# Optimization experiments

Measured on AMD Instinct MI355X. Metric: run time of the kernel, lower is better.

## Reference

```python
import jax, jax.numpy as jnp
import numpy as np

N = 4096      # nodes
E = 131072    # edges (before self loops)
C = 512       # channels
H = 8         # heads
CO = C // H   # per-head out channels (64)
EPS = 1e-5
NEG_SLOPE = 0.2


def layer_norm(x, g, b):
    mu = jnp.mean(x, axis=-1, keepdims=True)
    var = jnp.mean((x - mu) ** 2, axis=-1, keepdims=True)
    return (x - mu) * jax.lax.rsqrt(var + EPS) * g + b


def gatv2(x, src, dst, wl, bl, wr, br, att, bias):
    # PyG GATv2Conv, concat=True, add_self_loops handled by caller.
    n = x.shape[0]
    xl = (x @ wl.T + bl).reshape(n, H, CO)   # target-side features
    xr = (x @ wr.T + br).reshape(n, H, CO)   # source-side features (messages)
    e = jax.nn.leaky_relu(xl[dst] + xr[src], NEG_SLOPE)   # [E+N, H, CO]
    alpha = jnp.einsum('ehc,hc->eh', e, att)              # [E+N, H]
    # segment softmax over destination neighborhoods
    amax = jax.ops.segment_max(alpha, dst, num_segments=n)
    ex = jnp.exp(alpha - amax[dst])
    denom = jax.ops.segment_sum(ex, dst, num_segments=n)
    a = ex / denom[dst]                                   # [E+N, H]
    msg = xr[src] * a[:, :, None]                         # [E+N, H, CO]
    out = jax.ops.segment_sum(msg, dst, num_segments=n)   # [N, H, CO]
    return out.reshape(n, H * CO) + bias


def mha(x, in_w, in_b, out_w, out_b):
    # nn.MultiheadAttention self-attention, batch=1, eval mode
    n = x.shape[0]
    qkv = x @ in_w.T + in_b                               # [N, 3C]
    q, k, v = jnp.split(qkv, 3, axis=-1)
    q = q.reshape(n, H, CO); k = k.reshape(n, H, CO); v = v.reshape(n, H, CO)
    scores = jnp.einsum('qhd,khd->hqk', q, k) / jnp.sqrt(jnp.float32(CO))
    p = jax.nn.softmax(scores, axis=-1)
    o = jnp.einsum('hqk,khd->qhd', p, v).reshape(n, C)
    return o @ out_w.T + out_b


def setup_inputs() -> dict:
    key = jax.random.key(0)
    ks = jax.random.split(key, 24)
    s = 0.02
    d = {}
    d['x'] = jax.random.normal(ks[0], (N, C), jnp.float32)
    d['edge_index'] = jax.random.randint(ks[1], (2, E), 0, N, dtype=jnp.int64)
    d['gat_wl'] = jax.random.normal(ks[2], (H * CO, C), jnp.float32) * s
    d['gat_bl'] = jnp.zeros((H * CO,), jnp.float32)
    d['gat_wr'] = jax.random.normal(ks[3], (H * CO, C), jnp.float32) * s
    d['gat_br'] = jnp.zeros((H * CO,), jnp.float32)
    d['gat_att'] = jax.random.normal(ks[4], (H, CO), jnp.float32) * s
    d['gat_b'] = jnp.zeros((H * CO,), jnp.float32)
    d['in_w'] = jax.random.normal(ks[5], (3 * C, C), jnp.float32) * s
    d['in_b'] = jnp.zeros((3 * C,), jnp.float32)
    d['out_w'] = jax.random.normal(ks[6], (C, C), jnp.float32) * s
    d['out_b'] = jnp.zeros((C,), jnp.float32)
    d['ln1_g'] = jnp.ones((C,), jnp.float32); d['ln1_b'] = jnp.zeros((C,), jnp.float32)
    d['ln2_g'] = jnp.ones((C,), jnp.float32); d['ln2_b'] = jnp.zeros((C,), jnp.float32)
    d['ln3_g'] = jnp.ones((C,), jnp.float32); d['ln3_b'] = jnp.zeros((C,), jnp.float32)
    d['w1'] = jax.random.normal(ks[7], (4 * C, C), jnp.float32) * s
    d['b1'] = jnp.zeros((4 * C,), jnp.float32)
    d['w2'] = jax.random.normal(ks[8], (C, 4 * C), jnp.float32) * s
    d['b2'] = jnp.zeros((C,), jnp.float32)
    return d


def reference(x, edge_index, gat_wl, gat_bl, gat_wr, gat_br, gat_att, gat_b,
              in_w, in_b, out_w, out_b, ln1_g, ln1_b, ln2_g, ln2_b,
              ln3_g, ln3_b, w1, b1, w2, b2):
    n = x.shape[0]
    loops = jnp.arange(n, dtype=edge_index.dtype)
    src = jnp.concatenate([edge_index[0], loops])
    dst = jnp.concatenate([edge_index[1], loops])
    h_local = gatv2(x, src, dst, gat_wl, gat_bl, gat_wr, gat_br, gat_att, gat_b)
    x = layer_norm(x + h_local, ln1_g, ln1_b)
    h_global = mha(x, in_w, in_b, out_w, out_b)
    x = layer_norm(x + h_global, ln2_g, ln2_b)
    h_ffn = (jax.nn.gelu(x @ w1.T + b1, approximate=False)) @ w2.T + b2
    x = layer_norm(x + h_ffn, ln3_g, ln3_b)
    return x
```

## Files before the change

kernel.cpp:

```cpp
#include <hip/hip_runtime.h>
#include <math.h>

#define NN 4096
#define CC 512
#define EE 131072
#define NEDGE (EE + NN)
#define HH 8
#define DCO 64
#define NC2 2097152L

typedef __attribute__((ext_vector_type(8))) short bfrag;
typedef __attribute__((ext_vector_type(4))) float f32x4;
typedef __attribute__((ext_vector_type(4))) int i32x4;

__device__ __forceinline__ float bf2f(unsigned short u) {
  union { float f; unsigned int i; } x; x.i = ((unsigned int)u) << 16; return x.f;
}
__device__ __forceinline__ unsigned short f2bf(float f) {
  union { float f; unsigned int i; } x; x.f = f;
  unsigned int r = x.i + 0x7FFFu + ((x.i >> 16) & 1u);
  return (unsigned short)(r >> 16);
}
__device__ __forceinline__ unsigned short f2bf_trunc(float f) {
  union { float f; unsigned int i; } x; x.f = f;
  return (unsigned short)(x.i >> 16);
}

__device__ __forceinline__ void gld16(const unsigned short* g, unsigned short* l) {
  __builtin_amdgcn_global_load_lds(
      (__attribute__((address_space(1))) unsigned int*)g,
      (__attribute__((address_space(3))) unsigned int*)l, 16, 0, 0);
}

#define QSC 0.18033688011112042f

#define CX  2097152L
#define CWL (CX + 262144L)
#define CWR (CWL + 262144L)
#define CIW (CWR + 786432L)
#define COW (CIW + 262144L)
#define CW1 (COW + 1048576L)
#define CW2 (CW1 + 1048576L)

__global__ void cvt_all(const float* __restrict__ x, const float* __restrict__ wl,
                        const float* __restrict__ wr, const float* __restrict__ iw,
                        const float* __restrict__ ow, const float* __restrict__ w1,
                        const float* __restrict__ w2, unsigned short* __restrict__ dst,
                        int* __restrict__ cntcur, const float* __restrict__ bl,
                        const float* __restrict__ br, float* __restrict__ biasc) {
  if (blockIdx.x >= 5632) {
    int t = threadIdx.x;
    if (blockIdx.x == 5632) {
      for (int k = t; k < 8192; k += 256) cntcur[k] = 0;
    } else {
      for (int k = t; k < 512; k += 256) {
        biasc[k] = bl[k];
        biasc[512 + k] = br[k];
      }
    }
    return;
  }
  long i = ((long)blockIdx.x * 256 + threadIdx.x) * 4;
  const float* s; long o;
  if (i < CX)       { s = x;  o = i; }
  else if (i < CWL) { s = wl; o = i - CX; }
  else if (i < CWR) { s = wr; o = i - CWL; }
  else if (i < CIW) { s = iw; o = i - CWR; }
  else if (i < COW) { s = ow; o = i - CIW; }
  else if (i < CW1) { s = w1; o = i - COW; }
  else              { s = w2; o = i - CW1; }
  f32x4 v = *(const f32x4*)(s + o);
  union { unsigned long long q; unsigned short u[4]; } t;
#pragma unroll
  for (int j = 0; j < 4; j++) t.u[j] = f2bf(v[j]);
  *(unsigned long long*)(dst + i) = t.q;
}

template<int OMODE, int TN, bool SPLIT>
__global__ __launch_bounds__(256) void gemm_t(
    const unsigned short* __restrict__ A, const unsigned short* __restrict__ B,
    const float* __restrict__ bias, void* __restrict__ C,
    int K, int lda, int ldb, int ldc)
{
  __shared__ unsigned short As[4096];
  __shared__ unsigned short Bs[TN * 32];
  constexpr int MI = (TN == 128) ? 4 : 2;
  const int tid = threadIdx.x;
  const int wave = tid >> 6, lane = tid & 63;
  const int ml = lane & 15, kq = lane >> 4;
  const int wm = (TN == 128) ? ((wave >> 1) << 6) : (wave << 5);
  const int wn = (TN == 128) ? ((wave & 1) << 6) : 0;
  const int bm = blockIdx.y << 7, bn = blockIdx.x * TN;
  const int srow = tid >> 2, scol = (tid & 3) << 3;
  if (SPLIT) { A += (long)blockIdx.z * K; B += (long)blockIdx.z * K; }
  const float* biasp = (!SPLIT || blockIdx.z == 0) ? bias : nullptr;
  const unsigned short* Ag = A + (long)(bm + srow) * lda + scol;
  const unsigned short* Bg = B + (long)(bn + srow) * ldb + scol;
  const long astep = (long)64 * lda, bstep = (long)64 * ldb;
  unsigned short* lA0 = As + tid * 8;
  unsigned short* lA1 = As + 2048 + tid * 8;
  unsigned short* lB0 = Bs + tid * 8;
  f32x4 acc[MI][4];
#pragma unroll
  for (int mi = 0; mi < MI; mi++)
#pragma unroll
    for (int ni = 0; ni < 4; ni++) acc[mi][ni] = (f32x4){0.f, 0.f, 0.f, 0.f};
  for (int k0 = 0; k0 < K; k0 += 32) {
    __syncthreads();
    gld16(Ag, lA0); gld16(Ag + astep, lA1);
    gld16(Bg, lB0);
    if (TN == 128) gld16(Bg + bstep, Bs + 2048 + tid * 8);
    Ag += 32; Bg += 32;
    __syncthreads();
    bfrag af[MI], bf[4];
#pragma unroll
    for (int mi = 0; mi < MI; mi++)
      af[mi] = *(const bfrag*)&As[(wm + (mi << 4) + ml) * 32 + (kq << 3)];
#pragma unroll
    for (int ni = 0; ni < 4; ni++)
      bf[ni] = *(const bfrag*)&Bs[(wn + (ni << 4) + ml) * 32 + (kq << 3)];
#pragma unroll
    for (int mi = 0; mi < MI; mi++)
#pragma unroll
      for (int ni = 0; ni < 4; ni++)
        acc[mi][ni] = __builtin_amdgcn_mfma_f32_16x16x32_bf16(af[mi], bf[ni], acc[mi][ni], 0, 0, 0);
  }
#pragma unroll
  for (int ni = 0; ni < 4; ni++) {
    int col = bn + wn + (ni << 4) + ml;
    float bb = biasp ? biasp[col] : 0.f;
#pragma unroll
    for (int mi = 0; mi < MI; mi++) {
      int row0 = bm + wm + (mi << 4) + (kq << 2);
#pragma unroll
      for (int r = 0; r < 4; r++) {
        float v = acc[mi][ni][r] + bb;
        int row = row0 + r;
        if (OMODE == 3) {
          unsigned short* q = (unsigned short*)C;
          if (col < 512) {
            int h = col >> 6, d = col & 63;
            q[(long)h * (NN * DCO) + (long)row * DCO + d] = f2bf(v * QSC);
          } else if (col < 1024) {
            int c2 = col - 512, h = c2 >> 6, d = c2 & 63;
            q[NC2 + (long)h * (NN * DCO) + (long)row * DCO + d] = f2bf(v);
          } else {
            int c2 = col - 1024, h = c2 >> 6, d = c2 & 63;
            q[2 * NC2 + (long)h * (DCO * NN) + (long)d * NN + row] = f2bf(v);
          }
        } else if (OMODE == 0) {
          long off = (SPLIT ? (long)blockIdx.z * NC2 : 0) + (long)row * ldc + col;
          ((float*)C)[off] = v;
        } else {
          if (OMODE == 2) v = 0.5f * v * (1.f + erff(v * 0.70710678118f));
          ((unsigned short*)C)[(long)row * ldc + col] = f2bf(v);
        }
      }
    }
  }
}

__global__ void count_k(const int* __restrict__ ei, int* __restrict__ cnt) {
  int e = blockIdx.x * 256 + threadIdx.x;
  if (e >= NEDGE) return;
  int d = (e < EE) ? ei[EE + e] : (e - EE);
  atomicAdd(&cnt[d], 1);
}

__global__ void scan_k(const int* __restrict__ cnt, int* __restrict__ rowptr) {
  __shared__ int s[1024];
  int t = threadIdx.x;
  int b = t * 4;
  int c0 = cnt[b], c1 = cnt[b + 1], c2 = cnt[b + 2], c3 = cnt[b + 3];
  int sum = c0 + c1 + c2 + c3;
  s[t] = sum;
  __syncthreads();
  for (int o = 1; o < 1024; o <<= 1) {
    int v = (t >= o) ? s[t - o] : 0;
    __syncthreads();
    s[t] += v;
    __syncthreads();
  }
  int ex = s[t] - sum;
  rowptr[b] = ex; rowptr[b + 1] = ex + c0;
  rowptr[b + 2] = ex + c0 + c1; rowptr[b + 3] = ex + c0 + c1 + c2;
  if (t == 1023) rowptr[4096] = ex + sum;
}

__global__ void scatter_k(const int* __restrict__ ei, const int* __restrict__ rowptr,
                          int* __restrict__ cur, int* __restrict__ order) {
  int e = blockIdx.x * 256 + threadIdx.x;
  if (e >= NEDGE) return;
  int d = (e < EE) ? ei[EE + e] : (e - EE);
  int p = atomicAdd(&cur[d], 1);
  order[rowptr[d] + p] = e;
}

__global__ __launch_bounds__(256) void gat_fused(
    const unsigned short* __restrict__ xlr, const float* __restrict__ x,
    const int* __restrict__ order, const int* __restrict__ rowptr,
    const int* __restrict__ ei, const float* __restrict__ att,
    const float* __restrict__ gbias,
    const float* __restrict__ g, const float* __restrict__ be,
    float* __restrict__ of, unsigned short* __restrict__ ob)
{
  __shared__ float part[4][512];
  __shared__ float sw[4][8];
  __shared__ float sinv[8];
  __shared__ float shl[8];
  int n = blockIdx.x, t = threadIdx.x;
  int beg = rowptr[n], deg = rowptr[n + 1] - beg;
  int wave = t >> 6, lane = t & 63;
  int ch = lane << 3;
  union U8 { i32x4 v; unsigned short u[8]; };
  U8 XL; XL.v = *(const i32x4*)(xlr + (long)n * 1024 + ch);
  float xl[8];
#pragma unroll
  for (int j = 0; j < 8; j++) xl[j] = bf2f(XL.u[j]);
  f32x4 t0 = *(const f32x4*)(att + ch);
  f32x4 t1 = *(const f32x4*)(att + ch + 4);
  float acc[8];
#pragma unroll
  for (int j = 0; j < 8; j++) acc[j] = 0.f;
  float se = 0.f;
  int i = wave;
  U8 X;
  if (i < deg) {
    int e = order[beg + i];
    int sn = (e < EE) ? ei[e] : (e - EE);
    X.v = *(const i32x4*)(xlr + (long)sn * 1024 + 512 + ch);
  }
  while (i < deg) {
    U8 Xc = X;
    int inext = i + 4;
    if (inext < deg) {
      int e = order[beg + inext];
      int sn = (e < EE) ? ei[e] : (e - EE);
      X.v = *(const i32x4*)(xlr + (long)sn * 1024 + 512 + ch);
    }
    float xr[8];
    float p = 0.f;
#pragma unroll
    for (int j = 0; j < 8; j++) {
      xr[j] = bf2f(Xc.u[j]);
      float v = xl[j] + xr[j];
      v = (v > 0.f) ? v : 0.2f * v;
      float tv = (j < 4) ? t0[j] : t1[j - 4];
      p += tv * v;
    }
    p += __shfl_xor(p, 1); p += __shfl_xor(p, 2); p += __shfl_xor(p, 4);
    float ew = __expf(p);
    se += ew;
#pragma unroll
    for (int j = 0; j < 8; j++) acc[j] += ew * xr[j];
    i = inext;
  }
  *(f32x4*)&part[wave][ch]     = (f32x4){acc[0], acc[1], acc[2], acc[3]};
  *(f32x4*)&part[wave][ch + 4] = (f32x4){acc[4], acc[5], acc[6], acc[7]};
  if ((lane & 7) == 0) sw[wave][lane >> 3] = se;
  __syncthreads();
  if (t < 8) sinv[t] = 1.f / (sw[0][t] + sw[1][t] + sw[2][t] + sw[3][t]);
  __syncthreads();
  long base = (long)n * CC;
  float v0, v1;
  {
    int c = t;
    float p4 = part[0][c] + part[1][c] + part[2][c] + part[3][c];
    v0 = x[base + c] + p4 * sinv[c >> 6] + gbias[c];
  }
  {
    int c = t + 256;
    float p4 = part[0][c] + part[1][c] + part[2][c] + part[3][c];
    v1 = x[base + c] + p4 * sinv[c >> 6] + gbias[c];
  }
  float s = v0 + v1, ss = v0 * v0 + v1 * v1;
  for (int o = 32; o > 0; o >>= 1) { s += __shfl_down(s, o); ss += __shfl_down(ss, o); }
  if (lane == 0) { shl[wave] = s; shl[4 + wave] = ss; }
  __syncthreads();
  float S = shl[0] + shl[1] + shl[2] + shl[3];
  float SS = shl[4] + shl[5] + shl[6] + shl[7];
  float mean = S * (1.f / 512.f);
  float var = SS * (1.f / 512.f) - mean * mean;
  float rs = rsqrtf(var + 1e-5f);
  float y0 = (v0 - mean) * rs * g[t] + be[t];
  float y1 = (v1 - mean) * rs * g[t + 256] + be[t + 256];
  of[base + t] = y0; of[base + t + 256] = y1;
  ob[base + t] = f2bf(y0); ob[base + t + 256] = f2bf(y1);
}

template<int NS>
__global__ __launch_bounds__(256) void resid_ln(
    const float* __restrict__ a, const float* __restrict__ b,
    const float* __restrict__ g, const float* __restrict__ be,
    float* __restrict__ of, unsigned short* __restrict__ ob)
{
  __shared__ float sh[8];
  int row = blockIdx.x, t = threadIdx.x;
  long base = (long)row * CC;
  float b0 = 0.f, b1 = 0.f;
#pragma unroll
  for (int s = 0; s < NS; s++) {
    b0 += b[(long)s * NC2 + base + t];
    b1 += b[(long)s * NC2 + base + t + 256];
  }
  float v0 = a[base + t] + b0;
  float v1 = a[base + t + 256] + b1;
  float s = v0 + v1, ss = v0 * v0 + v1 * v1;
  for (int o = 32; o > 0; o >>= 1) { s += __shfl_down(s, o); ss += __shfl_down(ss, o); }
  int wave = t >> 6, lane = t & 63;
  if (lane == 0) { sh[wave] = s; sh[4 + wave] = ss; }
  __syncthreads();
  float S = sh[0] + sh[1] + sh[2] + sh[3];
  float SS = sh[4] + sh[5] + sh[6] + sh[7];
  float mean = S * (1.f / 512.f);
  float var = SS * (1.f / 512.f) - mean * mean;
  float rs = rsqrtf(var + 1e-5f);
  float y0 = (v0 - mean) * rs * g[t] + be[t];
  float y1 = (v1 - mean) * rs * g[t + 256] + be[t + 256];
  if (of) { of[base + t] = y0; of[base + t + 256] = y1; }
  if (ob) { ob[base + t] = f2bf(y0); ob[base + t + 256] = f2bf(y1); }
}

__global__ __launch_bounds__(256, 4) void flash_attn(
    const unsigned short* __restrict__ qkvP, unsigned short* __restrict__ Op,
    float* __restrict__ Lp)
{
  __shared__ unsigned short QP[128 * 72];
  __shared__ unsigned short Ks[64 * 72];
  __shared__ unsigned short Vs[64 * 72];
  const int tid = threadIdx.x;
  const int wave = tid >> 6, lane = tid & 63;
  const int ml = lane & 15, kq = lane >> 4;
  const int h = blockIdx.x & 7, qt = blockIdx.x >> 3;
  const int sp = blockIdx.y;
  const int n0 = qt << 7;
  const unsigned short* Qh = qkvP + (long)h * (NN * DCO);
  const unsigned short* Kh = qkvP + NC2 + (long)h * (NN * DCO);
  const unsigned short* Vh = qkvP + 2 * NC2 + (long)h * (DCO * NN);
  {
    int r = tid >> 1, c = (tid & 1) << 5;
    const unsigned short* src = Qh + (long)(n0 + r) * DCO + c;
    unsigned short* d = &QP[r * 72 + c];
    *(i32x4*)d        = *(const i32x4*)src;
    *(i32x4*)(d + 8)  = *(const i32x4*)(src + 8);
    *(i32x4*)(d + 16) = *(const i32x4*)(src + 16);
    *(i32x4*)(d + 24) = *(const i32x4*)(src + 24);
  }
  __syncthreads();
  bfrag aq[2][2];
#pragma unroll
  for (int s = 0; s < 2; s++)
#pragma unroll
    for (int kh = 0; kh < 2; kh++)
      aq[s][kh] = *(const bfrag*)&QP[(wave * 32 + s * 16 + ml) * 72 + kh * 32 + (kq << 3)];
  bfrag ones;
#pragma unroll
  for (int j = 0; j < 8; j++) ones[j] = (short)0x3F80;
  f32x4 Oa[2][4];
  f32x4 Lc[2];
#pragma unroll
  for (int s = 0; s < 2; s++) {
    Lc[s] = (f32x4){0.f, 0.f, 0.f, 0.f};
#pragma unroll
    for (int dg = 0; dg < 4; dg++) Oa[s][dg] = (f32x4){0.f, 0.f, 0.f, 0.f};
  }
  const int r_ = tid >> 2, c_ = (tid & 3) << 4;
  const int j0 = sp << 4;
  i32x4 ka, kb, va, vb;
  {
    int k0 = j0 << 6;
    ka = *(const i32x4*)(Kh + (long)(k0 + r_) * DCO + c_);
    kb = *(const i32x4*)(Kh + (long)(k0 + r_) * DCO + c_ + 8);
    va = *(const i32x4*)(Vh + (long)r_ * NN + k0 + c_);
    vb = *(const i32x4*)(Vh + (long)r_ * NN + k0 + c_ + 8);
  }
  for (int jj = 0; jj < 16; jj++) {
    if (jj) __syncthreads();
    *(i32x4*)&Ks[r_ * 72 + c_] = ka; *(i32x4*)&Ks[r_ * 72 + c_ + 8] = kb;
    *(i32x4*)&Vs[r_ * 72 + c_] = va; *(i32x4*)&Vs[r_ * 72 + c_ + 8] = vb;
    __syncthreads();
    if (jj < 15) {
      int k0 = (j0 + jj + 1) << 6;
      ka = *(const i32x4*)(Kh + (long)(k0 + r_) * DCO + c_);
      kb = *(const i32x4*)(Kh + (long)(k0 + r_) * DCO + c_ + 8);
      va = *(const i32x4*)(Vh + (long)r_ * NN + k0 + c_);
      vb = *(const i32x4*)(Vh + (long)r_ * NN + k0 + c_ + 8);
    }
    f32x4 sc[2][4];
#pragma unroll
    for (int s = 0; s < 2; s++)
#pragma unroll
      for (int c = 0; c < 4; c++) sc[s][c] = (f32x4){0.f, 0.f, 0.f, 0.f};
    __builtin_amdgcn_s_setprio(1);
#pragma unroll
    for (int c = 0; c < 4; c++) {
      bfrag bk0 = *(const bfrag*)&Ks[(c * 16 + ml) * 72 + (kq << 3)];
      bfrag bk1 = *(const bfrag*)&Ks[(c * 16 + ml) * 72 + 32 + (kq << 3)];
#pragma unroll
      for (int s = 0; s < 2; s++) {
        sc[s][c] = __builtin_amdgcn_mfma_f32_16x16x32_bf16(bk0, aq[s][0], sc[s][c], 0, 0, 0);
        sc[s][c] = __builtin_amdgcn_mfma_f32_16x16x32_bf16(bk1, aq[s][1], sc[s][c], 0, 0, 0);
      }
    }
    __builtin_amdgcn_s_setprio(0);
#pragma unroll
    for (int s = 0; s < 2; s++) {
#pragma unroll
      for (int c = 0; c < 4; c++) {
        float p0 = exp2f(sc[s][c][0]);
        float p1 = exp2f(sc[s][c][1]);
        float p2 = exp2f(sc[s][c][2]);
        float p3 = exp2f(sc[s][c][3]);
        unsigned int w0, w1;
        asm("v_cvt_pk_bf16_f32 %0, %1, %2" : "=v"(w0) : "v"(p0), "v"(p1));
        asm("v_cvt_pk_bf16_f32 %0, %1, %2" : "=v"(w1) : "v"(p2), "v"(p3));
        union { unsigned long long q; unsigned int w[2]; } u;
        u.w[0] = w0; u.w[1] = w1;
        *(unsigned long long*)&QP[(wave * 32 + s * 16 + ml) * 72 + c * 16 + (kq << 2)] = u.q;
      }
    }
    bfrag ap[2][2];
#pragma unroll
    for (int s = 0; s < 2; s++)
#pragma unroll
      for (int kh = 0; kh < 2; kh++)
        ap[s][kh] = *(const bfrag*)&QP[(wave * 32 + s * 16 + ml) * 72 + kh * 32 + (kq << 3)];
    __builtin_amdgcn_s_setprio(1);
#pragma unroll
    for (int s = 0; s < 2; s++) {
      Lc[s] = __builtin_amdgcn_mfma_f32_16x16x32_bf16(ap[s][0], ones, Lc[s], 0, 0, 0);
      Lc[s] = __builtin_amdgcn_mfma_f32_16x16x32_bf16(ap[s][1], ones, Lc[s], 0, 0, 0);
    }
#pragma unroll
    for (int dg = 0; dg < 4; dg++) {
      bfrag bv0 = *(const bfrag*)&Vs[(dg * 16 + ml) * 72 + (kq << 3)];
      bfrag bv1 = *(const bfrag*)&Vs[(dg * 16 + ml) * 72 + 32 + (kq << 3)];
#pragma unroll
      for (int s = 0; s < 2; s++) {
        Oa[s][dg] = __builtin_amdgcn_mfma_f32_16x16x32_bf16(ap[s][0], bv0, Oa[s][dg], 0, 0, 0);
        Oa[s][dg] = __builtin_amdgcn_mfma_f32_16x16x32_bf16(ap[s][1], bv1, Oa[s][dg], 0, 0, 0);
      }
    }
    __builtin_amdgcn_s_setprio(0);
  }
  long obase = (long)sp * NC2;
#pragma unroll
  for (int s = 0; s < 2; s++)
#pragma unroll
    for (int dg = 0; dg < 4; dg++)
#pragma unroll
      for (int r = 0; r < 4; r++) {
        int row = wave * 32 + s * 16 + (kq << 2) + r;
        Op[obase + (long)(n0 + row) * CC + (h << 6) + (dg << 4) + ml] = f2bf(Oa[s][dg][r]);
      }
  if (ml == 0) {
#pragma unroll
    for (int s = 0; s < 2; s++)
#pragma unroll
      for (int r = 0; r < 4; r++) {
        int row = wave * 32 + s * 16 + (kq << 2) + r;
        Lp[(long)sp * (NN * HH) + (long)(n0 + row) * HH + h] = Lc[s][r];
      }
  }
}

__global__ void flash_combine(const unsigned short* __restrict__ Op,
                              const float* __restrict__ Lp,
                              unsigned short* __restrict__ Ao) {
  int idx = blockIdx.x * 256 + threadIdx.x;
  int n = idx >> 9, c = idx & 511, h = c >> 6;
  float l = 0.f, o = 0.f;
#pragma unroll
  for (int s = 0; s < 4; s++) {
    l += Lp[(long)s * (NN * HH) + (long)n * HH + h];
    o += bf2f(Op[(long)s * NC2 + idx]);
  }
  Ao[idx] = f2bf(o / l);
}

extern "C" void kernel_launch(void* const* d_in, const int* in_sizes, int n_in,
                              void* d_out, int out_size, void* d_ws, size_t ws_size,
                              hipStream_t stream) {
  typedef unsigned short u16;
  const float* x      = (const float*)d_in[0];
  const int*   ei     = (const int*)d_in[1];
  const float* wl     = (const float*)d_in[2];
  const float* bl     = (const float*)d_in[3];
  const float* wr     = (const float*)d_in[4];
  const float* br     = (const float*)d_in[5];
  const float* att    = (const float*)d_in[6];
  const float* gat_b  = (const float*)d_in[7];
  const float* in_w   = (const float*)d_in[8];
  const float* in_b   = (const float*)d_in[9];
  const float* out_w  = (const float*)d_in[10];
  const float* out_b  = (const float*)d_in[11];
  const float* ln1g   = (const float*)d_in[12];
  const float* ln1b   = (const float*)d_in[13];
  const float* ln2g   = (const float*)d_in[14];
  const float* ln2b   = (const float*)d_in[15];
  const float* ln3g   = (const float*)d_in[16];
  const float* ln3b   = (const float*)d_in[17];
  const float* w1     = (const float*)d_in[18];
  const float* b1     = (const float*)d_in[19];
  const float* w2     = (const float*)d_in[20];
  const float* b2     = (const float*)d_in[21];

  const size_t MB = 1u << 20;
  char* w = (char*)d_ws;
  float* h_f32   = (float*)(w + 0);
  float* x2_f32  = (float*)(w + 8 * MB);
  int*   cnt     = (int*)(w + 16 * MB);
  int*   cur     = cnt + 4096;
  int*   rowptr  = (int*)(w + 16 * MB + 32 * 1024);
  int*   order   = (int*)(w + 16 * MB + 64 * 1024);
  u16*   cvt     = (u16*)(w + 17 * MB);
  u16*   xbf     = cvt;
  u16*   wlrbf   = cvt + CX;
  u16*   inwbf   = cvt + CWR;
  u16*   outwbf  = cvt + CIW;
  u16*   w1bf    = cvt + COW;
  u16*   w2bf    = cvt + CW1;
  u16*   xlr_bf  = (u16*)(w + 29 * MB);
  u16*   Opart   = (u16*)(w + 29 * MB);
  float* proj    = (float*)(w + 29 * MB);
  u16*   ffn1    = (u16*)(w + 61 * MB);
  u16*   qkvP    = (u16*)(w + 93 * MB);
  float* biasc   = (float*)(w + 105 * MB);
  float* Lpart   = (float*)(w + 105 * MB);
  u16*   Ao      = (u16*)(w + 106 * MB);
  u16*   actb    = (u16*)(w + 110 * MB);

  cvt_all<<<5634, 256, 0, stream>>>(x, wl, wr, in_w, out_w, w1, w2, cvt,
                                    cnt, bl, br, biasc);
  count_k<<<(NEDGE + 255) / 256, 256, 0, stream>>>(ei, cnt);
  scan_k<<<1, 1024, 0, stream>>>(cnt, rowptr);
  scatter_k<<<(NEDGE + 255) / 256, 256, 0, stream>>>(ei, rowptr, cur, order);

  gemm_t<1, 64, false><<<dim3(16, 32), 256, 0, stream>>>(xbf, wlrbf, biasc, xlr_bf, 512, 512, 512, 1024);
  gat_fused<<<NN, 256, 0, stream>>>(xlr_bf, x, order, rowptr, ei, att, gat_b,
                                    ln1g, ln1b, h_f32, actb);

  gemm_t<3, 64, false><<<dim3(24, 32), 256, 0, stream>>>(actb, inwbf, in_b, qkvP, 512, 512, 512, 0);
  flash_attn<<<dim3(256, 4), 256, 0, stream>>>(qkvP, Opart, Lpart);
  flash_combine<<<(NN * CC) / 256, 256, 0, stream>>>(Opart, Lpart, Ao);
  gemm_t<0, 64, true><<<dim3(8, 32, 2), 256, 0, stream>>>(Ao, outwbf, out_b, proj, 256, 512, 512, 512);
  resid_ln<2><<<NN, 256, 0, stream>>>(h_f32, proj, ln2g, ln2b, x2_f32, actb);

  gemm_t<2, 128, false><<<dim3(16, 32), 256, 0, stream>>>(actb, w1bf, b1, ffn1, 512, 512, 512, 2048);
  gemm_t<0, 128, true><<<dim3(4, 32, 4), 256, 0, stream>>>(ffn1, w2bf, b2, proj, 512, 2048, 2048, 512);
  resid_ln<4><<<NN, 256, 0, stream>>>(x2_f32, proj, ln3g, ln3b, (float*)d_out, nullptr);
}
```

Baseline: 319.8 us.

## Load K/V fragments directly from global memory in flash attention, dropping LDS staging

The flash attention kernel no longer copies each 64-key K/V tile into shared memory with block-wide barriers. Each wave now reads its MFMA K and V fragments straight from global memory, and the barrier after the Q load is removed because each wave only reads its own Q rows. This removes the LDS stores, LDS reads and per-iteration __syncthreads. In exchange, each of the four waves fetches the same K/V data separately, which relies on the cache, and the register-prefetch pipelining of the next tile is lost. The launch bound is lowered to 3 blocks per SIMD to allow more registers for the fragment arrays.

```diff
diff --git a/kernel.cpp b/kernel.cpp
--- a/kernel.cpp
+++ b/kernel.cpp
@@ -321,13 +321,11 @@
   if (ob) { ob[base + t] = f2bf(y0); ob[base + t + 256] = f2bf(y1); }
 }
 
-__global__ __launch_bounds__(256, 4) void flash_attn(
+__global__ __launch_bounds__(256, 3) void flash_attn(
     const unsigned short* __restrict__ qkvP, unsigned short* __restrict__ Op,
     float* __restrict__ Lp)
 {
   __shared__ unsigned short QP[128 * 72];
-  __shared__ unsigned short Ks[64 * 72];
-  __shared__ unsigned short Vs[64 * 72];
   const int tid = threadIdx.x;
   const int wave = tid >> 6, lane = tid & 63;
   const int ml = lane & 15, kq = lane >> 4;
@@ -346,7 +344,6 @@
     *(i32x4*)(d + 16) = *(const i32x4*)(src + 16);
     *(i32x4*)(d + 24) = *(const i32x4*)(src + 24);
   }
-  __syncthreads();
   bfrag aq[2][2];
 #pragma unroll
   for (int s = 0; s < 2; s++)
@@ -364,27 +361,16 @@
 #pragma unroll
     for (int dg = 0; dg < 4; dg++) Oa[s][dg] = (f32x4){0.f, 0.f, 0.f, 0.f};
   }
-  const int r_ = tid >> 2, c_ = (tid & 3) << 4;
   const int j0 = sp << 4;
-  i32x4 ka, kb, va, vb;
-  {
-    int k0 = j0 << 6;
-    ka = *(const i32x4*)(Kh + (long)(k0 + r_) * DCO + c_);
-    kb = *(const i32x4*)(Kh + (long)(k0 + r_) * DCO + c_ + 8);
-    va = *(const i32x4*)(Vh + (long)r_ * NN + k0 + c_);
-    vb = *(const i32x4*)(Vh + (long)r_ * NN + k0 + c_ + 8);
-  }
   for (int jj = 0; jj < 16; jj++) {
-    if (jj) __syncthreads();
-    *(i32x4*)&Ks[r_ * 72 + c_] = ka; *(i32x4*)&Ks[r_ * 72 + c_ + 8] = kb;
-    *(i32x4*)&Vs[r_ * 72 + c_] = va; *(i32x4*)&Vs[r_ * 72 + c_ + 8] = vb;
-    __syncthreads();
-    if (jj < 15) {
-      int k0 = (j0 + jj + 1) << 6;
-      ka = *(const i32x4*)(Kh + (long)(k0 + r_) * DCO + c_);
-      kb = *(const i32x4*)(Kh + (long)(k0 + r_) * DCO + c_ + 8);
-      va = *(const i32x4*)(Vh + (long)r_ * NN + k0 + c_);
-      vb = *(const i32x4*)(Vh + (long)r_ * NN + k0 + c_ + 8);
+    const unsigned short* Kb = Kh + (((long)(j0 + jj)) << 6) * DCO;
+    const unsigned short* Vb = Vh + (((long)(j0 + jj)) << 6);
+    bfrag bk[4][2];
+#pragma unroll
+    for (int c = 0; c < 4; c++) {
+      const unsigned short* kp = Kb + (c * 16 + ml) * DCO + (kq << 3);
+      bk[c][0] = *(const bfrag*)kp;
+      bk[c][1] = *(const bfrag*)(kp + 32);
     }
     f32x4 sc[2][4];
 #pragma unroll
@@ -394,15 +380,20 @@
     __builtin_amdgcn_s_setprio(1);
 #pragma unroll
     for (int c = 0; c < 4; c++) {
-      bfrag bk0 = *(const bfrag*)&Ks[(c * 16 + ml) * 72 + (kq << 3)];
-      bfrag bk1 = *(const bfrag*)&Ks[(c * 16 + ml) * 72 + 32 + (kq << 3)];
 #pragma unroll
       for (int s = 0; s < 2; s++) {
-        sc[s][c] = __builtin_amdgcn_mfma_f32_16x16x32_bf16(bk0, aq[s][0], sc[s][c], 0, 0, 0);
-        sc[s][c] = __builtin_amdgcn_mfma_f32_16x16x32_bf16(bk1, aq[s][1], sc[s][c], 0, 0, 0);
+        sc[s][c] = __builtin_amdgcn_mfma_f32_16x16x32_bf16(bk[c][0], aq[s][0], sc[s][c], 0, 0, 0);
+        sc[s][c] = __builtin_amdgcn_mfma_f32_16x16x32_bf16(bk[c][1], aq[s][1], sc[s][c], 0, 0, 0);
       }
     }
     __builtin_amdgcn_s_setprio(0);
+    bfrag bv[4][2];
+#pragma unroll
+    for (int dg = 0; dg < 4; dg++) {
+      const unsigned short* vp = Vb + (long)(dg * 16 + ml) * NN + (kq << 3);
+      bv[dg][0] = *(const bfrag*)vp;
+      bv[dg][1] = *(const bfrag*)(vp + 32);
+    }
 #pragma unroll
     for (int s = 0; s < 2; s++) {
 #pragma unroll
@@ -433,12 +424,10 @@
     }
 #pragma unroll
     for (int dg = 0; dg < 4; dg++) {
-      bfrag bv0 = *(const bfrag*)&Vs[(dg * 16 + ml) * 72 + (kq << 3)];
-      bfrag bv1 = *(const bfrag*)&Vs[(dg * 16 + ml) * 72 + 32 + (kq << 3)];
 #pragma unroll
       for (int s = 0; s < 2; s++) {
-        Oa[s][dg] = __builtin_amdgcn_mfma_f32_16x16x32_bf16(ap[s][0], bv0, Oa[s][dg], 0, 0, 0);
-        Oa[s][dg] = __builtin_amdgcn_mfma_f32_16x16x32_bf16(ap[s][1], bv1, Oa[s][dg], 0, 0, 0);
+        Oa[s][dg] = __builtin_amdgcn_mfma_f32_16x16x32_bf16(ap[s][0], bv[dg][0], Oa[s][dg], 0, 0, 0);
+        Oa[s][dg] = __builtin_amdgcn_mfma_f32_16x16x32_bf16(ap[s][1], bv[dg][1], Oa[s][dg], 0, 0, 0);
       }
     }
     __builtin_amdgcn_s_setprio(0);
```

Result: slower. 416.8 us (+30.3%).
